# Kernel optimization log

Hardware: AMD Instinct MI355X
Metric: run time of the kernel (lower is better)

## Reference

```python
import jax, jax.numpy as jnp
import numpy as np
from jax import lax

H = 64  # hidden_size == embedding_size


def gru_last_hidden(emb, W_ih, W_hh, b_ih, b_hh):
    """PyTorch single-layer GRU over seq [L, H]; returns final hidden [H].
    Gate order in stacked weights: r, z, n (PyTorch convention)."""
    def step(h, x):
        gi = W_ih @ x + b_ih            # [3H]
        gh = W_hh @ h + b_hh            # [3H]
        i_r, i_z, i_n = jnp.split(gi, 3)
        h_r, h_z, h_n = jnp.split(gh, 3)
        r = jax.nn.sigmoid(i_r + h_r)
        z = jax.nn.sigmoid(i_z + h_z)
        n = jnp.tanh(i_n + r * h_n)
        h_new = (1.0 - z) * n + z * h
        return h_new, None
    h0 = jnp.zeros((H,), dtype=emb.dtype)
    h_last, _ = lax.scan(step, h0, emb)
    return h_last


def setup_inputs() -> dict:
    key = jax.random.key(0)
    ks = jax.random.split(key, 12)
    N, D, A, V, L = 256, 128, 40, 128, 16
    F3_IN = N * (D + H + N)
    s = 0.02
    return {
        "obs": jax.random.normal(ks[0], (N, D), dtype=jnp.float32),
        "token_ids": jax.random.randint(ks[1], (L,), 0, V),
        "emb_table": jax.random.normal(ks[2], (V, H), dtype=jnp.float32) * s,
        "gru_Wih": jax.random.normal(ks[3], (3 * H, H), dtype=jnp.float32) * s,
        "gru_Whh": jax.random.normal(ks[4], (3 * H, H), dtype=jnp.float32) * s,
        "gru_bih": jnp.zeros((3 * H,), dtype=jnp.float32),
        "gru_bhh": jnp.zeros((3 * H,), dtype=jnp.float32),
        "f1_W": jax.random.normal(ks[5], (H, 2 * D), dtype=jnp.float32) * s,
        "f1_b": jnp.zeros((H,), dtype=jnp.float32),
        "f3_W1": jax.random.normal(ks[6], (512, F3_IN), dtype=jnp.float32) * s,
        "f3_b1": jnp.zeros((512,), dtype=jnp.float32),
        "f3_W2": jax.random.normal(ks[7], (A, 512), dtype=jnp.float32) * s,
        "f3_b2": jnp.zeros((A,), dtype=jnp.float32),
    }


def reference(obs, token_ids, emb_table, gru_Wih, gru_Whh, gru_bih, gru_bhh,
              f1_W, f1_b, f3_W1, f3_b1, f3_W2, f3_b2):
    N = obs.shape[0]
    # Encoder: embedding lookup + GRU, keep last timestep output
    emb = emb_table[token_ids]                       # [L, H]
    g_tilde = gru_last_hidden(emb, gru_Wih, gru_Whh, gru_bih, gru_bhh)  # [H]

    # Pairwise f1 + dot with g_tilde. f1(concat(o_i,o_j)) @ g = obs_i@Wa.T@g
    # + obs_j@Wb.T@g + b@g  (exact factorization of the linear over pairs).
    Wa, Wb = jnp.split(f1_W, 2, axis=1)              # each [H, D]
    u = obs @ (Wa.T @ g_tilde)                       # [N]  (outer index a)
    v = obs @ (Wb.T @ g_tilde)                       # [N]  (inner index b)
    Z = u[:, None] + v[None, :] + jnp.dot(f1_b, g_tilde)   # [N, N]

    # softmax over ALL N^2 entries (torch Softmax(dim=0) on the flat stack)
    p = jax.nn.softmax(Z.reshape(-1)).reshape(N, N)

    g_rep = jnp.broadcast_to(g_tilde, (N, H))
    x = jnp.concatenate([obs, g_rep, p], axis=1).reshape(-1)  # [N*(D+H+N)]

    h1 = jax.nn.relu(f3_W1 @ x + f3_b1)
    return f3_W2 @ h1 + f3_b2                         # [action_shape]
```

## Files before the change

### kernel.cpp

```cpp
#include <hip/hip_runtime.h>
#include <math.h>

#define H    64
#define N    256
#define D    128
#define L    16
#define SEG4   112
#define F3IN (N * 448)
#define CG4   1792

typedef float v4f __attribute__((ext_vector_type(4)));

__device__ __forceinline__ float sigmoidf_(float x) {
    return 1.0f / (1.0f + expf(-x));
}
__device__ __forceinline__ float dot4(float4 a, float4 b) {
    return a.x * b.x + a.y * b.y + a.z * b.z + a.w * b.w;
}
__device__ __forceinline__ float dotv(v4f a, v4f b) {
    return a[0] * b[0] + a[1] * b[1] + a[2] * b[2] + a[3] * b[3];
}

__global__ __launch_bounds__(256, 1) void k_enc(
    const int* __restrict__ token_ids, const float* __restrict__ emb_table,
    const float* __restrict__ Wih, const float* __restrict__ Whh,
    const float* __restrict__ bih, const float* __restrict__ bhh,
    const float* __restrict__ f1W, const float* __restrict__ obs,
    float* __restrict__ g_out, float* __restrict__ eus_out,
    float* __restrict__ ev_out)
{
    __shared__ float emb_s[L * H];
    __shared__ float gi_all[L * 192];
    __shared__ float h_s[H];
    __shared__ float gh_s[192];
    __shared__ float wa_s[D];
    __shared__ float wb_s[D];
    __shared__ float wred[4][4];

    const int k = threadIdx.x;
    const int wave = k >> 6, lane = k & 63;

    {
        int tok = token_ids[k >> 4];
        ((float4*)emb_s)[k] = ((const float4*)emb_table)[tok * 16 + (k & 15)];
    }
    if (k < H) h_s[k] = 0.0f;

    float4 wih4[16], whh4[16];
    float bi = 0.0f, bh = 0.0f;
    if (k < 192) {
        const float4* wi = (const float4*)(Wih + k * H);
        const float4* wh = (const float4*)(Whh + k * H);
#pragma unroll
        for (int c = 0; c < 16; ++c) { wih4[c] = wi[c]; whh4[c] = wh[c]; }
        bi = bih[k]; bh = bhh[k];
    }

    float f1wreg[64];
#pragma unroll
    for (int kk = 0; kk < 64; ++kk) f1wreg[kk] = f1W[kk * 256 + k];

    __syncthreads();

    if (k < 192) {
        float gi[L];
#pragma unroll
        for (int tt = 0; tt < L; ++tt) gi[tt] = bi;
#pragma unroll
        for (int c = 0; c < 16; ++c) {
            float4 w = wih4[c];
#pragma unroll
            for (int tt = 0; tt < L; ++tt)
                gi[tt] += dot4(w, ((const float4*)(emb_s + tt * 64))[c]);
        }
#pragma unroll
        for (int tt = 0; tt < L; ++tt) gi_all[tt * 192 + k] = gi[tt];
    }
    __syncthreads();

    for (int tt = 0; tt < L; ++tt) {
        if (k < 192) {
            const float4* hv = (const float4*)h_s;
            float a0 = 0, a1 = 0, a2 = 0, a3 = 0;
#pragma unroll
            for (int c = 0; c < 16; c += 4) {
                a0 += dot4(whh4[c],     hv[c]);
                a1 += dot4(whh4[c + 1], hv[c + 1]);
                a2 += dot4(whh4[c + 2], hv[c + 2]);
                a3 += dot4(whh4[c + 3], hv[c + 3]);
            }
            gh_s[k] = (a0 + a1) + (a2 + a3) + bh;
        }
        __syncthreads();
        if (k < H) {
            float r = sigmoidf_(gi_all[tt * 192 + k] + gh_s[k]);
            float z = sigmoidf_(gi_all[tt * 192 + 64 + k] + gh_s[64 + k]);
            float n = tanhf(gi_all[tt * 192 + 128 + k] + r * gh_s[128 + k]);
            h_s[k] = (1.0f - z) * n + z * h_s[k];
        }
        __syncthreads();
    }

    {
        float s = 0.0f;
#pragma unroll
        for (int kk = 0; kk < 64; ++kk) s += f1wreg[kk] * h_s[kk];
        if (k < D) wa_s[k] = s;
        else       wb_s[k - D] = s;
        if (k < H) g_out[k] = h_s[k];
    }
    __syncthreads();

    float4 orow[32];
    {
        const float4* rp = (const float4*)(obs + k * D);
#pragma unroll
        for (int c = 0; c < 32; ++c) orow[c] = rp[c];
    }
    float u = 0.0f, v = 0.0f;
#pragma unroll
    for (int c = 0; c < 32; ++c) {
        u += dot4(orow[c], ((const float4*)wa_s)[c]);
        v += dot4(orow[c], ((const float4*)wb_s)[c]);
    }

    float um = u, vm = v;
#pragma unroll
    for (int off = 32; off > 0; off >>= 1) {
        um = fmaxf(um, __shfl_xor(um, off, 64));
        vm = fmaxf(vm, __shfl_xor(vm, off, 64));
    }
    if (lane == 0) { wred[0][wave] = um; wred[1][wave] = vm; }
    __syncthreads();
    const float mu = fmaxf(fmaxf(wred[0][0], wred[0][1]), fmaxf(wred[0][2], wred[0][3]));
    const float mv = fmaxf(fmaxf(wred[1][0], wred[1][1]), fmaxf(wred[1][2], wred[1][3]));

    const float eui = expf(u - mu), evi = expf(v - mv);
    float us = eui, vs = evi;
#pragma unroll
    for (int off = 32; off > 0; off >>= 1) {
        us += __shfl_xor(us, off, 64);
        vs += __shfl_xor(vs, off, 64);
    }
    if (lane == 0) { wred[2][wave] = us; wred[3][wave] = vs; }
    __syncthreads();
    const float Su = (wred[2][0] + wred[2][1]) + (wred[2][2] + wred[2][3]);
    const float Sv = (wred[3][0] + wred[3][1]) + (wred[3][2] + wred[3][3]);

    eus_out[k] = eui * (1.0f / (Su * Sv));
    ev_out[k]  = evi;
}

__global__ __launch_bounds__(256, 4) void k_mv(
    const float* __restrict__ W1, const float* __restrict__ obs,
    const float* __restrict__ g, const float* __restrict__ eus,
    const float* __restrict__ ev, float* __restrict__ partial)
{
    const int t  = threadIdx.x;
    const int cg = blockIdx.x & 15;
    const int rg = blockIdx.x >> 4;
    const int wave = t >> 6, lane = t & 63;

    v4f xr[7];
    {
        const float4* obs4 = (const float4*)obs;
        const float4* g4   = (const float4*)g;
        const float4* ev4  = (const float4*)ev;
#pragma unroll
        for (int j = 0; j < 7; ++j) {
            int idx = wave * 448 + j * 64 + lane;
            int s   = idx / SEG4;
            int c   = idx - s * SEG4;
            int seg = cg * 16 + s;
            float4 o;
            if (c < 32)       o = obs4[seg * 32 + c];
            else if (c < 48)  o = g4[c - 32];
            else {
                float4 e = ev4[c - 48];
                float m = eus[seg];
                o = make_float4(e.x * m, e.y * m, e.z * m, e.w * m);
            }
            xr[j] = (v4f){o.x, o.y, o.z, o.w};
        }
    }

    const v4f* w0 = (const v4f*)W1 + (size_t)(rg * 2) * (F3IN / 4)
                  + (size_t)cg * CG4 + wave * 448 + lane;
    const v4f* w1 = w0 + (F3IN / 4);

    float s0a = 0.0f, s0b = 0.0f, s1a = 0.0f, s1b = 0.0f;
#pragma unroll
    for (int j = 0; j < 7; ++j) {
        v4f wa = w0[j * 64];
        v4f wb = w1[j * 64];
        float da = dotv(wa, xr[j]);
        float db = dotv(wb, xr[j]);
        if (j & 1) { s0b += da; s1b += db; }
        else       { s0a += da; s1a += db; }
    }
    float sums[2] = { s0a + s0b, s1a + s1b };

    __shared__ float red[2][4];
#pragma unroll
    for (int rr = 0; rr < 2; ++rr) {
        float s = sums[rr];
#pragma unroll
        for (int off = 32; off > 0; off >>= 1) s += __shfl_down(s, off, 64);
        if (lane == 0) red[rr][wave] = s;
    }
    __syncthreads();
    if (t < 2)
        partial[(rg * 2 + t) * 16 + cg] =
            red[t][0] + red[t][1] + red[t][2] + red[t][3];
}

__global__ __launch_bounds__(512) void k_finish(
    const float* __restrict__ partial, const float* __restrict__ b1,
    const float* __restrict__ W2, const float* __restrict__ b2,
    float* __restrict__ out)
{
    __shared__ float h1s[512];
    const int r = threadIdx.x;
    {
        const float4* p4 = (const float4*)(partial + r * 16);
        float4 A = p4[0], B = p4[1], C = p4[2], E = p4[3];
        float s = (A.x + A.y + A.z + A.w) + (B.x + B.y + B.z + B.w)
                + (C.x + C.y + C.z + C.w) + (E.x + E.y + E.z + E.w);
        h1s[r] = fmaxf(s + b1[r], 0.0f);
    }
    __syncthreads();

    const int wave = r >> 6, lane = r & 63;
    for (int row = wave; row < 40; row += 8) {
        float s = 0.0f;
#pragma unroll
        for (int c = 0; c < 8; ++c)
            s += W2[row * 512 + lane + c * 64] * h1s[lane + c * 64];
#pragma unroll
        for (int off = 32; off > 0; off >>= 1) s += __shfl_down(s, off, 64);
        if (lane == 0) out[row] = s + b2[row];
    }
}

extern "C" void kernel_launch(void* const* d_in, const int* in_sizes, int n_in,
                              void* d_out, int out_size, void* d_ws, size_t ws_size,
                              hipStream_t stream)
{
    const float* obs       = (const float*)d_in[0];
    const int*   token_ids = (const int*)  d_in[1];
    const float* emb_table = (const float*)d_in[2];
    const float* Wih       = (const float*)d_in[3];
    const float* Whh       = (const float*)d_in[4];
    const float* bih       = (const float*)d_in[5];
    const float* bhh       = (const float*)d_in[6];
    const float* f1W       = (const float*)d_in[7];
    const float* W1        = (const float*)d_in[9];
    const float* b1        = (const float*)d_in[10];
    const float* W2        = (const float*)d_in[11];
    const float* b2        = (const float*)d_in[12];

    float* ws      = (float*)d_ws;
    float* g       = ws;
    float* eus     = ws + 64;
    float* ev      = ws + 320;
    float* partial = ws + 640;
    float* out     = (float*)d_out;

    k_enc<<<1, 256, 0, stream>>>(token_ids, emb_table, Wih, Whh, bih, bhh,
                                 f1W, obs, g, eus, ev);
    k_mv<<<4096, 256, 0, stream>>>(W1, obs, g, eus, ev, partial);
    k_finish<<<1, 512, 0, stream>>>(partial, b1, W2, b2, out);
}
```

Baseline: 73.58 us.

## Fuse encoder into matvec kernel, recomputing GRU per block with 16 rows each

Merges the single-block encoder kernel into the W1 matvec kernel. Each of 512 blocks now recomputes the GRU, softmax statistics and the x vector in shared memory, then handles 16 output rows instead of 2. This removes a kernel launch, the serial single-block encoder phase and the global round trip for g/eus/ev. The cost is redundant encoder work in every block, plus register pressure from 16 accumulators and the launch bound changing to 2 blocks per CU, which may reduce the memory-level parallelism available for streaming the 58 MB W1.

```diff
diff --git a/kernel.cpp b/kernel.cpp
--- a/kernel.cpp
+++ b/kernel.cpp
@@ -21,13 +21,12 @@
     return a[0] * b[0] + a[1] * b[1] + a[2] * b[2] + a[3] * b[3];
 }
 
-__global__ __launch_bounds__(256, 1) void k_enc(
+__global__ __launch_bounds__(256, 2) void k_mega(
     const int* __restrict__ token_ids, const float* __restrict__ emb_table,
     const float* __restrict__ Wih, const float* __restrict__ Whh,
     const float* __restrict__ bih, const float* __restrict__ bhh,
     const float* __restrict__ f1W, const float* __restrict__ obs,
-    float* __restrict__ g_out, float* __restrict__ eus_out,
-    float* __restrict__ ev_out)
+    const float* __restrict__ W1, float* __restrict__ partial)
 {
     __shared__ float emb_s[L * H];
     __shared__ float gi_all[L * 192];
@@ -35,7 +34,10 @@
     __shared__ float gh_s[192];
     __shared__ float wa_s[D];
     __shared__ float wb_s[D];
+    __shared__ float eus_s[N];
+    __shared__ float ev_s[N];
     __shared__ float wred[4][4];
+    __shared__ float red[16][4];
 
     const int k = threadIdx.x;
     const int wave = k >> 6, lane = k & 63;
@@ -46,13 +48,12 @@
     }
     if (k < H) h_s[k] = 0.0f;
 
-    float4 wih4[16], whh4[16];
+    float4 whh4[16];
     float bi = 0.0f, bh = 0.0f;
     if (k < 192) {
-        const float4* wi = (const float4*)(Wih + k * H);
         const float4* wh = (const float4*)(Whh + k * H);
 #pragma unroll
-        for (int c = 0; c < 16; ++c) { wih4[c] = wi[c]; whh4[c] = wh[c]; }
+        for (int c = 0; c < 16; ++c) whh4[c] = wh[c];
         bi = bih[k]; bh = bhh[k];
     }
 
@@ -66,9 +67,10 @@
         float gi[L];
 #pragma unroll
         for (int tt = 0; tt < L; ++tt) gi[tt] = bi;
+        const float4* wi = (const float4*)(Wih + k * H);
 #pragma unroll
         for (int c = 0; c < 16; ++c) {
-            float4 w = wih4[c];
+            float4 w = wi[c];
 #pragma unroll
             for (int tt = 0; tt < L; ++tt)
                 gi[tt] += dot4(w, ((const float4*)(emb_s + tt * 64))[c]);
@@ -107,7 +109,6 @@
         for (int kk = 0; kk < 64; ++kk) s += f1wreg[kk] * h_s[kk];
         if (k < D) wa_s[k] = s;
         else       wb_s[k - D] = s;
-        if (k < H) g_out[k] = h_s[k];
     }
     __syncthreads();
 
@@ -147,25 +148,16 @@
     const float Su = (wred[2][0] + wred[2][1]) + (wred[2][2] + wred[2][3]);
     const float Sv = (wred[3][0] + wred[3][1]) + (wred[3][2] + wred[3][3]);
 
-    eus_out[k] = eui * (1.0f / (Su * Sv));
-    ev_out[k]  = evi;
-}
-
-__global__ __launch_bounds__(256, 4) void k_mv(
-    const float* __restrict__ W1, const float* __restrict__ obs,
-    const float* __restrict__ g, const float* __restrict__ eus,
-    const float* __restrict__ ev, float* __restrict__ partial)
-{
-    const int t  = threadIdx.x;
-    const int cg = blockIdx.x & 15;
-    const int rg = blockIdx.x >> 4;
-    const int wave = t >> 6, lane = t & 63;
+    eus_s[k] = eui * (1.0f / (Su * Sv));
+    ev_s[k]  = evi;
+    __syncthreads();
+
+    const int cg   = blockIdx.x & 15;
+    const int rgrp = blockIdx.x >> 4;
 
     v4f xr[7];
     {
         const float4* obs4 = (const float4*)obs;
-        const float4* g4   = (const float4*)g;
-        const float4* ev4  = (const float4*)ev;
 #pragma unroll
         for (int j = 0; j < 7; ++j) {
             int idx = wave * 448 + j * 64 + lane;
@@ -174,44 +166,49 @@
             int seg = cg * 16 + s;
             float4 o;
             if (c < 32)       o = obs4[seg * 32 + c];
-            else if (c < 48)  o = g4[c - 32];
+            else if (c < 48)  o = ((const float4*)h_s)[c - 32];
             else {
-                float4 e = ev4[c - 48];
-                float m = eus[seg];
+                float4 e = ((const float4*)ev_s)[c - 48];
+                float m = eus_s[seg];
                 o = make_float4(e.x * m, e.y * m, e.z * m, e.w * m);
             }
             xr[j] = (v4f){o.x, o.y, o.z, o.w};
         }
     }
 
-    const v4f* w0 = (const v4f*)W1 + (size_t)(rg * 2) * (F3IN / 4)
+    const v4f* w0 = (const v4f*)W1 + (size_t)(rgrp * 16) * (F3IN / 4)
                   + (size_t)cg * CG4 + wave * 448 + lane;
-    const v4f* w1 = w0 + (F3IN / 4);
-
-    float s0a = 0.0f, s0b = 0.0f, s1a = 0.0f, s1b = 0.0f;
-#pragma unroll
-    for (int j = 0; j < 7; ++j) {
-        v4f wa = w0[j * 64];
-        v4f wb = w1[j * 64];
-        float da = dotv(wa, xr[j]);
-        float db = dotv(wb, xr[j]);
-        if (j & 1) { s0b += da; s1b += db; }
-        else       { s0a += da; s1a += db; }
-    }
-    float sums[2] = { s0a + s0b, s1a + s1b };
-
-    __shared__ float red[2][4];
-#pragma unroll
-    for (int rr = 0; rr < 2; ++rr) {
+    float sums[16];
+#pragma unroll
+    for (int rp = 0; rp < 8; ++rp) {
+        const v4f* wra = w0 + (size_t)(2 * rp) * (F3IN / 4);
+        const v4f* wrb = wra + (F3IN / 4);
+        float s0a = 0, s0b = 0, s1a = 0, s1b = 0;
+#pragma unroll
+        for (int j = 0; j < 7; ++j) {
+            v4f wa = wra[j * 64];
+            v4f wb = wrb[j * 64];
+            float da = dotv(wa, xr[j]);
+            float db = dotv(wb, xr[j]);
+            if (j & 1) { s0b += da; s1b += db; }
+            else       { s0a += da; s1a += db; }
+        }
+        sums[2 * rp]     = s0a + s0b;
+        sums[2 * rp + 1] = s1a + s1b;
+    }
+
+    __syncthreads();
+#pragma unroll
+    for (int rr = 0; rr < 16; ++rr) {
         float s = sums[rr];
 #pragma unroll
         for (int off = 32; off > 0; off >>= 1) s += __shfl_down(s, off, 64);
         if (lane == 0) red[rr][wave] = s;
     }
     __syncthreads();
-    if (t < 2)
-        partial[(rg * 2 + t) * 16 + cg] =
-            red[t][0] + red[t][1] + red[t][2] + red[t][3];
+    if (k < 16)
+        partial[(rgrp * 16 + k) * 16 + cg] =
+            red[k][0] + red[k][1] + red[k][2] + red[k][3];
 }
 
 __global__ __launch_bounds__(512) void k_finish(
@@ -260,14 +257,10 @@
     const float* b2        = (const float*)d_in[12];
 
     float* ws      = (float*)d_ws;
-    float* g       = ws;
-    float* eus     = ws + 64;
-    float* ev      = ws + 320;
-    float* partial = ws + 640;
+    float* partial = ws;
     float* out     = (float*)d_out;
 
-    k_enc<<<1, 256, 0, stream>>>(token_ids, emb_table, Wih, Whh, bih, bhh,
-                                 f1W, obs, g, eus, ev);
-    k_mv<<<4096, 256, 0, stream>>>(W1, obs, g, eus, ev, partial);
+    k_mega<<<512, 256, 0, stream>>>(token_ids, emb_table, Wih, Whh, bih, bhh,
+                                    f1W, obs, W1, partial);
     k_finish<<<1, 512, 0, stream>>>(partial, b1, W2, b2, out);
 }
```

Result: slower. 130.5 us (+77.4%).
